# Kernel tuning notes

Hardware: AMD Instinct MI355X
Metric: run time of the kernel (lower is better)

The kernel has to match this reference:

```python
import jax, jax.numpy as jnp
import numpy as np

N_NODES = 30000
N_EDGES = 480000
IN_FEAT = 256
OUT_FEAT = 256
N_RELS = 8
N_HEADS = 4
HEAD_DIM = OUT_FEAT // N_HEADS
LEAKY_SLOPE = 0.2


def setup_inputs() -> dict:
    key = jax.random.key(0)
    ks = jax.random.split(key, 8)
    inputs = jax.random.normal(ks[0], (N_NODES, IN_FEAT), dtype=jnp.float32)
    conv_weights = jax.random.normal(ks[1], (N_RELS, N_HEADS, IN_FEAT, HEAD_DIM), dtype=jnp.float32) * (1.0 / np.sqrt(IN_FEAT))
    attn_l = jax.random.normal(ks[2], (N_RELS, N_HEADS, HEAD_DIM), dtype=jnp.float32) * 0.1
    attn_r = jax.random.normal(ks[3], (N_RELS, N_HEADS, HEAD_DIM), dtype=jnp.float32) * 0.1
    h_bias = jax.random.normal(ks[4], (OUT_FEAT,), dtype=jnp.float32) * 0.02
    edge_src = jax.random.randint(ks[5], (N_EDGES,), 0, N_NODES, dtype=jnp.int32)
    edge_dst = jax.random.randint(ks[6], (N_EDGES,), 0, N_NODES, dtype=jnp.int32)
    edge_type = jax.random.randint(ks[7], (N_EDGES,), 0, N_RELS, dtype=jnp.int32)
    return {"inputs": inputs, "conv_weights": conv_weights, "attn_l": attn_l,
            "attn_r": attn_r, "h_bias": h_bias, "edge_src": edge_src,
            "edge_dst": edge_dst, "edge_type": edge_type}


def reference(inputs, conv_weights, attn_l, attn_r, h_bias, edge_src, edge_dst, edge_type):
    # Per-relation dense transform of all node features: [R, N, H, D]
    feat_all = jnp.einsum('ni,rhid->rnhd', inputs, conv_weights)
    # Gather transformed source/destination features per edge: [E, H, D]
    feat_src_e = feat_all[edge_type, edge_src]
    feat_dst_e = feat_all[edge_type, edge_dst]
    # Per-edge attention logits (relation-specific attn vectors): [E, H]
    el = jnp.sum(feat_src_e * attn_l[edge_type], axis=-1)
    er = jnp.sum(feat_dst_e * attn_r[edge_type], axis=-1)
    e = jax.nn.leaky_relu(el + er, negative_slope=LEAKY_SLOPE)
    # Segment softmax over incoming edges of each destination node
    m = jax.ops.segment_max(e, edge_dst, num_segments=N_NODES)  # [N, H]
    ex = jnp.exp(e - m[edge_dst])
    denom = jax.ops.segment_sum(ex, edge_dst, num_segments=N_NODES)  # [N, H]
    alpha = ex / denom[edge_dst]  # [E, H]
    # Attention-weighted aggregation of transformed source features
    h = jax.ops.segment_sum(alpha[..., None] * feat_src_e, edge_dst, num_segments=N_NODES)  # [N, H, D]
    h = h.reshape(N_NODES, OUT_FEAT) + h_bias
    # activation=None, self_loop=False, dropout=0.0 (eval) -> identity
    return h
```

## Files before the change

kernel.cpp:

```cpp
#include <hip/hip_runtime.h>

#define N_NODES 30000
#define NPAD    30080
#define N_EDGES 480000
#define N_RELS  8
#define NB_SCAN 118

typedef short bf16x8 __attribute__((ext_vector_type(8)));
typedef float f32x4  __attribute__((ext_vector_type(4)));

__device__ __forceinline__ unsigned short f2bf(float f) {
    unsigned u = __float_as_uint(f);
    u += 0x7fffu + ((u >> 16) & 1u);
    return (unsigned short)(u >> 16);
}
__device__ __forceinline__ float bf2f(unsigned short h) {
    return __uint_as_float(((unsigned)h) << 16);
}

__device__ __forceinline__ void load_lds16(const void* g, void* l) {
    __builtin_amdgcn_global_load_lds(
        (const __attribute__((address_space(1))) unsigned int*)g,
        (__attribute__((address_space(3))) unsigned int*)l,
        16, 0, 0);
}

__global__ void prep_kernel(const float* __restrict__ x, unsigned short* __restrict__ xbf,
                            const float* __restrict__ cw, unsigned short* __restrict__ wt,
                            const int* __restrict__ edst, int* __restrict__ counts) {
    int b = blockIdx.x;
    if (b < 3760) {
        int t = b * 256 + threadIdx.x;
        int base = t * 8;
        int n = base >> 8;
        unsigned short h[8];
        if (n < N_NODES) {
            float4 a = *(const float4*)(x + base);
            float4 c = *(const float4*)(x + base + 4);
            h[0]=f2bf(a.x); h[1]=f2bf(a.y); h[2]=f2bf(a.z); h[3]=f2bf(a.w);
            h[4]=f2bf(c.x); h[5]=f2bf(c.y); h[6]=f2bf(c.z); h[7]=f2bf(c.w);
        } else {
            #pragma unroll
            for (int i = 0; i < 8; ++i) h[i] = 0;
        }
        uint4 o;
        o.x = (unsigned)h[0] | ((unsigned)h[1] << 16);
        o.y = (unsigned)h[2] | ((unsigned)h[3] << 16);
        o.z = (unsigned)h[4] | ((unsigned)h[5] << 16);
        o.w = (unsigned)h[6] | ((unsigned)h[7] << 16);
        *(uint4*)(xbf + base) = o;
    } else if (b < 5808) {
        int o = (b - 3760) * 256 + threadIdx.x;
        int i = o & 255;
        int c = (o >> 8) & 255;
        int r = o >> 16;
        float v = cw[(((size_t)r * 4 + (c >> 6)) * 256 + i) * 64 + (c & 63)];
        wt[o] = f2bf(v);
    } else {
        int e = (b - 5808) * 256 + threadIdx.x;
        if (e < N_EDGES) atomicAdd(&counts[edst[e]], 1);
    }
}

__global__ void scan1_kernel(const int* __restrict__ counts, int* __restrict__ locexcl,
                             int* __restrict__ bsum) {
    __shared__ int sm[256];
    int tid = threadIdx.x;
    int idx = blockIdx.x * 256 + tid;
    int v = (idx < N_NODES) ? counts[idx] : 0;
    sm[tid] = v;
    __syncthreads();
    for (int o = 1; o < 256; o <<= 1) {
        int t = (tid >= o) ? sm[tid - o] : 0;
        __syncthreads();
        sm[tid] += t;
        __syncthreads();
    }
    int incl = sm[tid];
    if (idx < N_NODES) locexcl[idx] = incl - v;
    if (tid == 255) bsum[blockIdx.x] = incl;
}

__global__ void scan2_kernel(const int* __restrict__ bsum, int* __restrict__ bpre) {
    __shared__ int sm[128];
    int tid = threadIdx.x;
    int v = (tid < NB_SCAN) ? bsum[tid] : 0;
    sm[tid] = v;
    __syncthreads();
    for (int o = 1; o < 128; o <<= 1) {
        int t = (tid >= o) ? sm[tid - o] : 0;
        __syncthreads();
        sm[tid] += t;
        __syncthreads();
    }
    if (tid < NB_SCAN) bpre[tid] = sm[tid] - v;
}

__global__ void scan3_kernel(const int* __restrict__ locexcl, const int* __restrict__ bpre,
                             int* __restrict__ offsets, int* __restrict__ cursor) {
    int idx = blockIdx.x * 256 + threadIdx.x;
    if (idx < N_NODES) {
        int o = bpre[blockIdx.x] + locexcl[idx];
        offsets[idx] = o;
        cursor[idx]  = o;
    }
    if (idx == 0) offsets[N_NODES] = N_EDGES;
}

__global__ __launch_bounds__(256) void gemm_kernel(
    const unsigned short* __restrict__ xbf,
    const unsigned short* __restrict__ wt,
    const float* __restrict__ attn_l,
    const float* __restrict__ attn_r,
    unsigned short* __restrict__ feat,
    float* __restrict__ projl,
    float* __restrict__ projr)
{
    __shared__ __align__(16) unsigned char smem[32768];

    const int tid  = threadIdx.x;
    const int lane = tid & 63;
    const int w    = tid >> 6;
    const int wm   = w >> 1;
    const int wn   = w & 1;
    const int quad = lane >> 4;
    const int l15  = lane & 15;

    const int bid = blockIdx.x;
    const int mt  = bid >> 4;
    const int r   = (bid >> 1) & 7;
    const int nt  = bid & 1;
    const int mbase = mt * 128;
    const int nbase = nt * 128;

    const unsigned short* Asrc = xbf + (size_t)mbase * 256;
    const unsigned short* Bsrc = wt + ((size_t)r * 256 + nbase) * 256;

    f32x4 acc[4][4] = {};

    const int srow = w * 16 + (lane >> 2);
    const int c0   = lane & 3;

    for (int k0 = 0; k0 < 256; k0 += 32) {
        #pragma unroll
        for (int n = 0; n < 2; ++n) {
            int row = n * 64 + srow;
            int c   = c0 ^ ((row >> 1) & 3);
            load_lds16(Asrc + (size_t)row * 256 + k0 + c * 8, smem + (n * 256 + w * 64) * 16);
        }
        #pragma unroll
        for (int n = 0; n < 2; ++n) {
            int row = n * 64 + srow;
            int c   = c0 ^ ((row >> 1) & 3);
            load_lds16(Bsrc + (size_t)row * 256 + k0 + c * 8, smem + 8192 + (n * 256 + w * 64) * 16);
        }
        __syncthreads();

        bf16x8 xf[4], wf[4];
        #pragma unroll
        for (int j = 0; j < 4; ++j) {
            int row = wm * 64 + j * 16 + l15;
            int cc  = quad ^ ((row >> 1) & 3);
            xf[j] = *(const bf16x8*)(smem + row * 64 + cc * 16);
        }
        #pragma unroll
        for (int i = 0; i < 4; ++i) {
            int row = wn * 64 + i * 16 + l15;
            int cc  = quad ^ ((row >> 1) & 3);
            wf[i] = *(const bf16x8*)(smem + 8192 + row * 64 + cc * 16);
        }

        #pragma unroll
        for (int i = 0; i < 4; ++i)
            #pragma unroll
            for (int j = 0; j < 4; ++j)
                acc[i][j] = __builtin_amdgcn_mfma_f32_16x16x32_bf16(wf[i], xf[j], acc[i][j], 0, 0, 0);
        __syncthreads();
    }

    #pragma unroll
    for (int j = 0; j < 4; ++j) {
        int node = mbase + wm * 64 + j * 16 + l15;
        size_t rowb = ((size_t)r * NPAD + node) * 256 + nbase + wn * 64;
        #pragma unroll
        for (int i = 0; i < 4; ++i) {
            ushort4 v;
            v.x = f2bf(acc[i][j][0]);
            v.y = f2bf(acc[i][j][1]);
            v.z = f2bf(acc[i][j][2]);
            v.w = f2bf(acc[i][j][3]);
            *(ushort4*)(feat + rowb + i * 16 + quad * 4) = v;
        }
    }

    const int head = nt * 2 + wn;
    float alv[4][4], arv[4][4];
    #pragma unroll
    for (int i = 0; i < 4; ++i)
        #pragma unroll
        for (int e = 0; e < 4; ++e) {
            int c = i * 16 + quad * 4 + e;
            alv[i][e] = attn_l[((size_t)r * 4 + head) * 64 + c];
            arv[i][e] = attn_r[((size_t)r * 4 + head) * 64 + c];
        }
    float* bufL = (float*)smem + w * 1024;
    float* bufR = (float*)(smem + 16384) + w * 1024;
    #pragma unroll
    for (int j = 0; j < 4; ++j) {
        float s1 = 0.f, s2 = 0.f;
        #pragma unroll
        for (int i = 0; i < 4; ++i)
            #pragma unroll
            for (int e = 0; e < 4; ++e) {
                s1 += acc[i][j][e] * alv[i][e];
                s2 += acc[i][j][e] * arv[i][e];
            }
        int node = j * 16 + l15;
        bufL[node * 5 + quad] = s1;
        bufR[node * 5 + quad] = s2;
    }
    float sL = 0.f, sR = 0.f;
    #pragma unroll
    for (int q = 0; q < 4; ++q) {
        sL += bufL[lane * 5 + q];
        sR += bufR[lane * 5 + q];
    }
    int g = mbase + wm * 64 + lane;
    projl[((size_t)r * NPAD + g) * 4 + head] = sL;
    projr[((size_t)r * NPAD + g) * 4 + head] = sR;
}

__global__ void logits_scatter_kernel(
    const int* __restrict__ esrc, const int* __restrict__ edst, const int* __restrict__ etyp,
    const float* __restrict__ projl, const float* __restrict__ projr,
    int* __restrict__ cursor, int* __restrict__ srcoff, float* __restrict__ exw)
{
    int e = blockIdx.x * 256 + threadIdx.x;
    if (e >= N_EDGES) return;
    int s = esrc[e], d = edst[e], t = etyp[e];
    float4 pl = ((const float4*)projl)[(size_t)t * NPAD + s];
    float4 pr = ((const float4*)projr)[(size_t)t * NPAD + d];
    float4 o;
    float v;
    v = pl.x + pr.x; v = v > 0.f ? v : 0.2f * v; o.x = __expf(v);
    v = pl.y + pr.y; v = v > 0.f ? v : 0.2f * v; o.y = __expf(v);
    v = pl.z + pr.z; v = v > 0.f ? v : 0.2f * v; o.z = __expf(v);
    v = pl.w + pr.w; v = v > 0.f ? v : 0.2f * v; o.w = __expf(v);
    int p = atomicAdd(&cursor[d], 1);
    srcoff[p] = t * NPAD + s;
    ((float4*)exw)[p] = o;
}

__global__ __launch_bounds__(256) void aggregate_kernel(
    const int* __restrict__ offsets, const int* __restrict__ srcoff,
    const float* __restrict__ exw, const unsigned short* __restrict__ feat,
    const float* __restrict__ bias, float* __restrict__ out)
{
    int v = blockIdx.x * 4 + (threadIdx.x >> 6);
    int lane = threadIdx.x & 63;
    int head = lane >> 4;
    int s0 = offsets[v], s1 = offsets[v + 1];
    float a0 = 0.f, a1 = 0.f, a2 = 0.f, a3 = 0.f, den = 0.f;
    int i = s0;
    for (; i + 8 <= s1; i += 8) {
        int o[8]; float ee[8]; ushort4 ff[8];
        #pragma unroll
        for (int u = 0; u < 8; ++u) { o[u] = srcoff[i + u]; ee[u] = exw[(size_t)(i + u) * 4 + head]; }
        #pragma unroll
        for (int u = 0; u < 8; ++u) ff[u] = *(const ushort4*)(feat + (size_t)o[u] * 256 + lane * 4);
        #pragma unroll
        for (int u = 0; u < 8; ++u) {
            den += ee[u];
            a0 += ee[u] * bf2f(ff[u].x);
            a1 += ee[u] * bf2f(ff[u].y);
            a2 += ee[u] * bf2f(ff[u].z);
            a3 += ee[u] * bf2f(ff[u].w);
        }
    }
    for (; i + 4 <= s1; i += 4) {
        int o[4]; float ee[4]; ushort4 ff[4];
        #pragma unroll
        for (int u = 0; u < 4; ++u) { o[u] = srcoff[i + u]; ee[u] = exw[(size_t)(i + u) * 4 + head]; }
        #pragma unroll
        for (int u = 0; u < 4; ++u) ff[u] = *(const ushort4*)(feat + (size_t)o[u] * 256 + lane * 4);
        #pragma unroll
        for (int u = 0; u < 4; ++u) {
            den += ee[u];
            a0 += ee[u] * bf2f(ff[u].x);
            a1 += ee[u] * bf2f(ff[u].y);
            a2 += ee[u] * bf2f(ff[u].z);
            a3 += ee[u] * bf2f(ff[u].w);
        }
    }
    for (; i + 2 <= s1; i += 2) {
        int o[2]; float ee[2]; ushort4 ff[2];
        #pragma unroll
        for (int u = 0; u < 2; ++u) { o[u] = srcoff[i + u]; ee[u] = exw[(size_t)(i + u) * 4 + head]; }
        #pragma unroll
        for (int u = 0; u < 2; ++u) ff[u] = *(const ushort4*)(feat + (size_t)o[u] * 256 + lane * 4);
        #pragma unroll
        for (int u = 0; u < 2; ++u) {
            den += ee[u];
            a0 += ee[u] * bf2f(ff[u].x);
            a1 += ee[u] * bf2f(ff[u].y);
            a2 += ee[u] * bf2f(ff[u].z);
            a3 += ee[u] * bf2f(ff[u].w);
        }
    }
    if (i < s1) {
        int o0 = srcoff[i];
        float e0 = exw[(size_t)i * 4 + head];
        ushort4 f0 = *(const ushort4*)(feat + (size_t)o0 * 256 + lane * 4);
        den += e0;
        a0 += e0 * bf2f(f0.x);
        a1 += e0 * bf2f(f0.y);
        a2 += e0 * bf2f(f0.z);
        a3 += e0 * bf2f(f0.w);
    }
    float inv = den > 0.f ? 1.f / den : 0.f;
    float4 o;
    o.x = a0 * inv + bias[lane * 4 + 0];
    o.y = a1 * inv + bias[lane * 4 + 1];
    o.z = a2 * inv + bias[lane * 4 + 2];
    o.w = a3 * inv + bias[lane * 4 + 3];
    ((float4*)out)[(size_t)v * 64 + lane] = o;
}

extern "C" void kernel_launch(void* const* d_in, const int* in_sizes, int n_in,
                              void* d_out, int out_size, void* d_ws, size_t ws_size,
                              hipStream_t stream) {
    const float* x    = (const float*)d_in[0];
    const float* cw   = (const float*)d_in[1];
    const float* al   = (const float*)d_in[2];
    const float* ar   = (const float*)d_in[3];
    const float* bias = (const float*)d_in[4];
    const int* esrc   = (const int*)d_in[5];
    const int* edst   = (const int*)d_in[6];
    const int* etyp   = (const int*)d_in[7];
    float* out        = (float*)d_out;

    char* ws = (char*)d_ws;
    size_t off = 0;
    auto alloc = [&](size_t bytes) { size_t o = off; off += (bytes + 255) & ~(size_t)255; return o; };

    unsigned short* xbf  = (unsigned short*)(ws + alloc((size_t)NPAD * 256 * 2));
    unsigned short* wt   = (unsigned short*)(ws + alloc((size_t)N_RELS * 256 * 256 * 2));
    unsigned short* feat = (unsigned short*)(ws + alloc((size_t)N_RELS * NPAD * 256 * 2));
    float* projl = (float*)(ws + alloc((size_t)N_RELS * NPAD * 4 * 4));
    float* projr = (float*)(ws + alloc((size_t)N_RELS * NPAD * 4 * 4));
    float* exw   = (float*)(ws + alloc((size_t)N_EDGES * 4 * 4));
    int* srcoff  = (int*)(ws + alloc((size_t)N_EDGES * 4));
    int* counts  = (int*)(ws + alloc((size_t)N_NODES * 4));
    int* offsets = (int*)(ws + alloc((size_t)(N_NODES + 1) * 4));
    int* cursor  = (int*)(ws + alloc((size_t)N_NODES * 4));
    int* locexcl = (int*)(ws + alloc((size_t)N_NODES * 4));
    int* bsum    = (int*)(ws + alloc((size_t)NB_SCAN * 4));
    int* bpre    = (int*)(ws + alloc((size_t)NB_SCAN * 4));

    hipMemsetAsync(counts, 0, (size_t)N_NODES * 4, stream);

    prep_kernel<<<7683, 256, 0, stream>>>(x, xbf, cw, wt, edst, counts);
    scan1_kernel<<<NB_SCAN, 256, 0, stream>>>(counts, locexcl, bsum);
    scan2_kernel<<<1, 128, 0, stream>>>(bsum, bpre);
    scan3_kernel<<<NB_SCAN, 256, 0, stream>>>(locexcl, bpre, offsets, cursor);
    gemm_kernel<<<3760, 256, 0, stream>>>(xbf, wt, al, ar, feat, projl, projr);
    logits_scatter_kernel<<<1875, 256, 0, stream>>>(esrc, edst, etyp, projl, projr,
                                                    cursor, srcoff, exw);
    aggregate_kernel<<<7500, 256, 0, stream>>>(offsets, srcoff, exw, feat, bias, out);
}
```

Baseline: 260.8 us.

## Split node aggregation across two wavefronts, remap GEMM blocks, use packed bf16 convert

The aggregate kernel now gives each destination node two wavefronts, each covering half of its incoming edges. Partial sums are combined through shared memory, which doubles the parallelism and shortens the per-wave dependency chain of the gather loop. The GEMM block index is remapped so consecutive blocks are spread across m-tiles (likely aimed at XCD/L2 locality), and the bf16 output conversion uses the packed intrinsic. The costs are a block-wide barrier, an LDS exchange, and half the waves sitting idle during the final write.

```diff
diff --git a/kernel.cpp b/kernel.cpp
--- a/kernel.cpp
+++ b/kernel.cpp
@@ -1,4 +1,5 @@
 #include <hip/hip_runtime.h>
+#include <hip/hip_bf16.h>
 
 #define N_NODES 30000
 #define NPAD    30080
@@ -16,6 +17,10 @@
 }
 __device__ __forceinline__ float bf2f(unsigned short h) {
     return __uint_as_float(((unsigned)h) << 16);
+}
+__device__ __forceinline__ ushort2 pk2bf(float a, float b) {
+    __hip_bfloat162 t = __float22bfloat162_rn(float2{a, b});
+    union { __hip_bfloat162 h; ushort2 u; } cv; cv.h = t; return cv.u;
 }
 
 __device__ __forceinline__ void load_lds16(const void* g, void* l) {
@@ -126,10 +131,11 @@
     const int quad = lane >> 4;
     const int l15  = lane & 15;
 
-    const int bid = blockIdx.x;
-    const int mt  = bid >> 4;
-    const int r   = (bid >> 1) & 7;
-    const int nt  = bid & 1;
+    const int bid  = blockIdx.x;
+    const int work = (bid & 7) * 470 + (bid >> 3);
+    const int mt   = work >> 4;
+    const int r    = (work >> 1) & 7;
+    const int nt   = work & 1;
     const int mbase = mt * 128;
     const int nbase = nt * 128;
 
@@ -184,11 +190,10 @@
         size_t rowb = ((size_t)r * NPAD + node) * 256 + nbase + wn * 64;
         #pragma unroll
         for (int i = 0; i < 4; ++i) {
+            ushort2 lo = pk2bf(acc[i][j][0], acc[i][j][1]);
+            ushort2 hi = pk2bf(acc[i][j][2], acc[i][j][3]);
             ushort4 v;
-            v.x = f2bf(acc[i][j][0]);
-            v.y = f2bf(acc[i][j][1]);
-            v.z = f2bf(acc[i][j][2]);
-            v.w = f2bf(acc[i][j][3]);
+            v.x = lo.x; v.y = lo.y; v.z = hi.x; v.w = hi.y;
             *(ushort4*)(feat + rowb + i * 16 + quad * 4) = v;
         }
     }
@@ -256,13 +261,20 @@
     const float* __restrict__ exw, const unsigned short* __restrict__ feat,
     const float* __restrict__ bias, float* __restrict__ out)
 {
-    int v = blockIdx.x * 4 + (threadIdx.x >> 6);
+    __shared__ float sm[2][64][5];
+    int wid  = threadIdx.x >> 6;
+    int slot = wid >> 1;
+    int half = wid & 1;
+    int v = blockIdx.x * 2 + slot;
     int lane = threadIdx.x & 63;
     int head = lane >> 4;
     int s0 = offsets[v], s1 = offsets[v + 1];
+    int mid = s0 + ((s1 - s0 + 1) >> 1);
+    int lo = half ? mid : s0;
+    int hi = half ? s1  : mid;
     float a0 = 0.f, a1 = 0.f, a2 = 0.f, a3 = 0.f, den = 0.f;
-    int i = s0;
-    for (; i + 8 <= s1; i += 8) {
+    int i = lo;
+    for (; i + 8 <= hi; i += 8) {
         int o[8]; float ee[8]; ushort4 ff[8];
         #pragma unroll
         for (int u = 0; u < 8; ++u) { o[u] = srcoff[i + u]; ee[u] = exw[(size_t)(i + u) * 4 + head]; }
@@ -277,7 +289,7 @@
             a3 += ee[u] * bf2f(ff[u].w);
         }
     }
-    for (; i + 4 <= s1; i += 4) {
+    for (; i + 4 <= hi; i += 4) {
         int o[4]; float ee[4]; ushort4 ff[4];
         #pragma unroll
         for (int u = 0; u < 4; ++u) { o[u] = srcoff[i + u]; ee[u] = exw[(size_t)(i + u) * 4 + head]; }
@@ -292,7 +304,7 @@
             a3 += ee[u] * bf2f(ff[u].w);
         }
     }
-    for (; i + 2 <= s1; i += 2) {
+    for (; i + 2 <= hi; i += 2) {
         int o[2]; float ee[2]; ushort4 ff[2];
         #pragma unroll
         for (int u = 0; u < 2; ++u) { o[u] = srcoff[i + u]; ee[u] = exw[(size_t)(i + u) * 4 + head]; }
@@ -307,7 +319,7 @@
             a3 += ee[u] * bf2f(ff[u].w);
         }
     }
-    if (i < s1) {
+    if (i < hi) {
         int o0 = srcoff[i];
         float e0 = exw[(size_t)i * 4 + head];
         ushort4 f0 = *(const ushort4*)(feat + (size_t)o0 * 256 + lane * 4);
@@ -317,13 +329,24 @@
         a2 += e0 * bf2f(f0.z);
         a3 += e0 * bf2f(f0.w);
     }
-    float inv = den > 0.f ? 1.f / den : 0.f;
-    float4 o;
-    o.x = a0 * inv + bias[lane * 4 + 0];
-    o.y = a1 * inv + bias[lane * 4 + 1];
-    o.z = a2 * inv + bias[lane * 4 + 2];
-    o.w = a3 * inv + bias[lane * 4 + 3];
-    ((float4*)out)[(size_t)v * 64 + lane] = o;
+    if (half) {
+        sm[slot][lane][0] = a0; sm[slot][lane][1] = a1;
+        sm[slot][lane][2] = a2; sm[slot][lane][3] = a3;
+        sm[slot][lane][4] = den;
+    }
+    __syncthreads();
+    if (!half) {
+        a0 += sm[slot][lane][0]; a1 += sm[slot][lane][1];
+        a2 += sm[slot][lane][2]; a3 += sm[slot][lane][3];
+        den += sm[slot][lane][4];
+        float inv = den > 0.f ? 1.f / den : 0.f;
+        float4 o;
+        o.x = a0 * inv + bias[lane * 4 + 0];
+        o.y = a1 * inv + bias[lane * 4 + 1];
+        o.z = a2 * inv + bias[lane * 4 + 2];
+        o.w = a3 * inv + bias[lane * 4 + 3];
+        ((float4*)out)[(size_t)v * 64 + lane] = o;
+    }
 }
 
 extern "C" void kernel_launch(void* const* d_in, const int* in_sizes, int n_in,
@@ -366,5 +389,5 @@
     gemm_kernel<<<3760, 256, 0, stream>>>(xbf, wt, al, ar, feat, projl, projr);
     logits_scatter_kernel<<<1875, 256, 0, stream>>>(esrc, edst, etyp, projl, projr,
                                                     cursor, srcoff, exw);
-    aggregate_kernel<<<7500, 256, 0, stream>>>(offsets, srcoff, exw, feat, bias, out);
-}
+    aggregate_kernel<<<15000, 256, 0, stream>>>(offsets, srcoff, exw, feat, bias, out);
+}
```

Result: no change. 258.2 us (-1.0%).
